# Optimization experiments

Hardware: AMD Instinct MI355X
Metric: run time of the kernel (lower is better)

## Reference

```python
import jax, jax.numpy as jnp
import numpy as np

B, T, H, L = 256, 1024, 64, 5  # batch, seq_len, hidden_size, num_layers


def setup_inputs() -> dict:
    key = jax.random.key(0)
    ks = jax.random.split(key, 10)
    s = 1.0 / np.sqrt(H)  # PyTorch LSTM/Linear uniform init bound

    def u(k, shape):
        return jax.random.uniform(k, shape, jnp.float32, -s, s)

    return {
        "x": jax.random.normal(ks[0], (B, T, 1), jnp.float32),
        "w_ih0": u(ks[1], (4 * H, 1)),          # layer 0 input weights (input_size=1)
        "w_ih_rest": u(ks[2], (L - 1, 4 * H, H)),  # layers 1..4 input weights
        "w_hh": u(ks[3], (L, 4 * H, H)),
        "b_ih": u(ks[4], (L, 4 * H)),
        "b_hh": u(ks[5], (L, 4 * H)),
        "W1": u(ks[6], (H, H)),
        "b1": u(ks[7], (H,)),
        "W2": u(ks[8], (1, H)),
        "b2": u(ks[9], (1,)),
        "future": 0,
    }


def _lstm_layer(x, w_ih, w_hh, b_ih, b_hh):
    # x: [B, T, in]; PyTorch gate order i, f, g, o
    gx = jnp.einsum('bti,gi->btg', x, w_ih) + b_ih  # precompute input projections [B,T,4H]
    h0 = jnp.zeros((x.shape[0], w_hh.shape[1]), x.dtype)

    def step(carry, gxt):
        h, c = carry
        gates = gxt + h @ w_hh.T + b_hh  # [B,4H]
        i, f, g, o = jnp.split(gates, 4, axis=-1)
        c = jax.nn.sigmoid(f) * c + jax.nn.sigmoid(i) * jnp.tanh(g)
        h = jax.nn.sigmoid(o) * jnp.tanh(c)
        return (h, c), h

    _, hs = jax.lax.scan(step, (h0, h0), jnp.swapaxes(gx, 0, 1))  # scan over time
    return jnp.swapaxes(hs, 0, 1)  # [B,T,H]


def _model(x, w_ih0, w_ih_rest, w_hh, b_ih, b_hh, W1, b1, W2, b2):
    # 5-layer LSTM (inter-layer dropout=0.1 is inactive in eval mode)
    h = _lstm_layer(x, w_ih0, w_hh[0], b_ih[0], b_hh[0])
    for l in range(1, w_hh.shape[0]):
        h = _lstm_layer(h, w_ih_rest[l - 1], w_hh[l], b_ih[l], b_hh[l])
    h = jax.nn.relu(h)
    h = jax.nn.relu(h @ W1.T + b1)
    return h @ W2.T + b2  # [B,T,1]


def reference(x, w_ih0, w_ih_rest, w_hh, b_ih, b_hh, W1, b1, W2, b2, future):
    out = None
    for _ in range(future + 1):
        out = _model(x, w_ih0, w_ih_rest, w_hh, b_ih, b_hh, W1, b1, W2, b2)
        x = jnp.concatenate([x, out[:, -1:, :]], axis=1)
    return out
```

## Files before the change

kernel.cpp:

```cpp
#include <hip/hip_runtime.h>

#define B_ 256
#define T_ 1024
#define H_ 64

typedef float f32x2 __attribute__((ext_vector_type(2)));
typedef float f32x4 __attribute__((ext_vector_type(4)));

__device__ __forceinline__ float fast_sigmoid(float x) {
    float e = __builtin_amdgcn_exp2f(-1.4426950408889634f * x);
    return __builtin_amdgcn_rcpf(1.0f + e);
}
__device__ __forceinline__ float fast_tanh(float x) {
    float e = __builtin_amdgcn_exp2f(2.8853900817779268f * x);
    return 1.0f - 2.0f * __builtin_amdgcn_rcpf(1.0f + e);
}

template<int CTRL>
__device__ __forceinline__ float dpp_addf(float v) {
    int vi = __builtin_bit_cast(int, v);
    int sh = __builtin_amdgcn_update_dpp(0, vi, CTRL, 0xF, 0xF, true);
    return v + __builtin_bit_cast(float, sh);
}

__device__ __forceinline__ f32x2 lo4(f32x4 v) { return __builtin_shufflevector(v, v, 0, 1); }
__device__ __forceinline__ f32x2 hi4(f32x4 v) { return __builtin_shufflevector(v, v, 2, 3); }

__device__ __forceinline__ void block_sync_lds() {
    asm volatile("s_waitcnt lgkmcnt(0)\n\ts_barrier" ::: "memory");
}

__device__ __forceinline__ float hsum4(f32x4 v) {
    return (v.x + v.y) + (v.z + v.w);
}

__device__ __forceinline__ void dot4x16(const f32x4 wt[4][4],
                                        f32x4 h0, f32x4 h1, f32x4 h2, f32x4 h3,
                                        float acc[4]) {
    #pragma unroll
    for (int r = 0; r < 4; ++r) {
        f32x2 a = {0.f, 0.f}, d = {0.f, 0.f};
        a = __builtin_elementwise_fma(lo4(wt[r][0]), lo4(h0), a);
        d = __builtin_elementwise_fma(hi4(wt[r][0]), hi4(h0), d);
        a = __builtin_elementwise_fma(lo4(wt[r][1]), lo4(h1), a);
        d = __builtin_elementwise_fma(hi4(wt[r][1]), hi4(h1), d);
        a = __builtin_elementwise_fma(lo4(wt[r][2]), lo4(h2), a);
        d = __builtin_elementwise_fma(hi4(wt[r][2]), hi4(h2), d);
        a = __builtin_elementwise_fma(lo4(wt[r][3]), lo4(h3), a);
        d = __builtin_elementwise_fma(hi4(wt[r][3]), hi4(h3), d);
        f32x2 s = a + d;
        acc[r] = s.x + s.y;
    }
}

__global__ __attribute__((amdgpu_flat_work_group_size(768, 768)))
void lstm_pair01(const float* __restrict__ xA,
                 float* __restrict__ hB_out,
                 const float* __restrict__ wA_ih,
                 const float* __restrict__ wA_hh,
                 const float* __restrict__ bA_ih,
                 const float* __restrict__ bA_hh,
                 const float* __restrict__ wB_ih,
                 const float* __restrict__ wB_hh,
                 const float* __restrict__ bB_ih,
                 const float* __restrict__ bB_hh)
{
    const int b   = blockIdx.x;
    const int tid = threadIdx.x;
    const bool isB = (tid < 512);

    __shared__ __align__(16) float xhA[2][80];
    __shared__ __align__(16) float xhB[2][160];

    int kc, j;
    f32x4 wt[4][4];
    float bias0 = 0.f, bias1 = 0.f, bias2 = 0.f, bias3 = 0.f;
    float w00 = 0.f, w01 = 0.f, w02 = 0.f, w03 = 0.f;

    if (isB) {
        kc = tid & 7; j = tid >> 3;
        #pragma unroll
        for (int r = 0; r < 4; ++r) {
            const int row = r * H_ + j;
            const float* base = (kc < 4) ? (wB_ih + row * H_ + kc * 16)
                                         : (wB_hh + row * H_ + (kc - 4) * 16);
            #pragma unroll
            for (int q = 0; q < 4; ++q) wt[r][q] = *(const f32x4*)(base + 4 * q);
        }
        if (kc == 0) {
            bias0 = bB_ih[0*H_+j] + bB_hh[0*H_+j];
            bias1 = bB_ih[1*H_+j] + bB_hh[1*H_+j];
            bias2 = bB_ih[2*H_+j] + bB_hh[2*H_+j];
            bias3 = bB_ih[3*H_+j] + bB_hh[3*H_+j];
        }
    } else {
        const int t2 = tid - 512;
        kc = t2 & 3; j = t2 >> 2;
        #pragma unroll
        for (int r = 0; r < 4; ++r) {
            const int row = r * H_ + j;
            const float* base = wA_hh + row * H_ + kc * 16;
            #pragma unroll
            for (int q = 0; q < 4; ++q) wt[r][q] = *(const f32x4*)(base + 4 * q);
        }
        if (kc == 0) {
            bias0 = bA_ih[0*H_+j] + bA_hh[0*H_+j];
            bias1 = bA_ih[1*H_+j] + bA_hh[1*H_+j];
            bias2 = bA_ih[2*H_+j] + bA_hh[2*H_+j];
            bias3 = bA_ih[3*H_+j] + bA_hh[3*H_+j];
            w00 = wA_ih[0*H_+j]; w01 = wA_ih[1*H_+j];
            w02 = wA_ih[2*H_+j]; w03 = wA_ih[3*H_+j];
        }
    }
    #pragma unroll
    for (int r = 0; r < 4; ++r)
        #pragma unroll
        for (int q = 0; q < 4; ++q)
            asm volatile("" : "+v"(wt[r][q]));

    float c_st = 0.f;
    float xt = (!isB) ? xA[(long)b * T_] : 0.f;

    if (isB) {
        if (tid < H_) xhB[1][80 + (tid >> 4) * 20 + (tid & 15)] = 0.f;
    } else {
        const int t2 = tid - 512;
        if (t2 < H_) xhA[0][(t2 >> 4) * 20 + (t2 & 15)] = 0.f;
    }
    block_sync_lds();

    for (int s = 0; s <= T_; ++s) {
        const int rb = s & 1, wb = rb ^ 1;

        if (isB) {
            if (s >= 1) {
                const f32x4* xv = (const f32x4*)&xhB[rb][kc * 20];
                f32x4 h0 = xv[0], h1 = xv[1], h2 = xv[2], h3 = xv[3];
                float acc[4];
                dot4x16(wt, h0, h1, h2, h3, acc);
                acc[0] = dpp_addf<0xB1>(acc[0]); acc[1] = dpp_addf<0xB1>(acc[1]);
                acc[2] = dpp_addf<0xB1>(acc[2]); acc[3] = dpp_addf<0xB1>(acc[3]);
                acc[0] = dpp_addf<0x4E>(acc[0]); acc[1] = dpp_addf<0x4E>(acc[1]);
                acc[2] = dpp_addf<0x4E>(acc[2]); acc[3] = dpp_addf<0x4E>(acc[3]);
                acc[0] = dpp_addf<0x141>(acc[0]); acc[1] = dpp_addf<0x141>(acc[1]);
                acc[2] = dpp_addf<0x141>(acc[2]); acc[3] = dpp_addf<0x141>(acc[3]);
                if (kc == 0) {
                    float i_ = fast_sigmoid(acc[0] + bias0);
                    float f_ = fast_sigmoid(acc[1] + bias1);
                    float g_ = fast_tanh   (acc[2] + bias2);
                    float o_ = fast_sigmoid(acc[3] + bias3);
                    c_st = f_ * c_st + i_ * g_;
                    float h = o_ * fast_tanh(c_st);
                    xhB[wb][80 + (j >> 4) * 20 + (j & 15)] = h;
                    hB_out[((long)b * T_ + (s - 1)) * H_ + j] = h;
                }
            }
        } else {
            if (s < T_) {
                float xn = 0.f;
                if (s + 1 < T_) xn = xA[(long)b * T_ + s + 1];
                const f32x4* xv = (const f32x4*)&xhA[rb][kc * 20];
                f32x4 h0 = xv[0], h1 = xv[1], h2 = xv[2], h3 = xv[3];
                float acc[4];
                dot4x16(wt, h0, h1, h2, h3, acc);
                acc[0] = dpp_addf<0xB1>(acc[0]); acc[1] = dpp_addf<0xB1>(acc[1]);
                acc[2] = dpp_addf<0xB1>(acc[2]); acc[3] = dpp_addf<0xB1>(acc[3]);
                acc[0] = dpp_addf<0x4E>(acc[0]); acc[1] = dpp_addf<0x4E>(acc[1]);
                acc[2] = dpp_addf<0x4E>(acc[2]); acc[3] = dpp_addf<0x4E>(acc[3]);
                if (kc == 0) {
                    float gi = acc[0] + bias0 + w00 * xt;
                    float gf = acc[1] + bias1 + w01 * xt;
                    float gg = acc[2] + bias2 + w02 * xt;
                    float go = acc[3] + bias3 + w03 * xt;
                    float i_ = fast_sigmoid(gi);
                    float f_ = fast_sigmoid(gf);
                    float g_ = fast_tanh(gg);
                    float o_ = fast_sigmoid(go);
                    c_st = f_ * c_st + i_ * g_;
                    float h = o_ * fast_tanh(c_st);
                    const int off = (j >> 4) * 20 + (j & 15);
                    xhA[wb][off] = h;
                    xhB[wb][off] = h;
                }
                xt = xn;
            }
        }
        block_sync_lds();
    }
}

__global__ __attribute__((amdgpu_flat_work_group_size(768, 768)))
void lstm_triple(const float* xin,
                 float* hout,
                 const float* __restrict__ wP_ih, const float* __restrict__ wP_hh,
                 const float* __restrict__ bP_ih, const float* __restrict__ bP_hh,
                 const float* __restrict__ wM_ih, const float* __restrict__ wM_hh,
                 const float* __restrict__ bM_ih, const float* __restrict__ bM_hh,
                 const float* __restrict__ wZ_ih, const float* __restrict__ wZ_hh,
                 const float* __restrict__ bZ_ih, const float* __restrict__ bZ_hh)
{
    const int b    = blockIdx.x;
    const int tid  = threadIdx.x;
    const int role = tid >> 8;
    const int loc  = tid & 255;
    const int kc   = loc & 3;
    const int j    = loc >> 2;

    __shared__ __align__(16) float bufP[2][144];
    __shared__ __align__(16) float bufM[2][144];
    __shared__ __align__(16) float bufZ[2][144];

    const float* w_ih = (role == 0) ? wP_ih : (role == 1) ? wM_ih : wZ_ih;
    const float* w_hh = (role == 0) ? wP_hh : (role == 1) ? wM_hh : wZ_hh;
    const float* b_ih = (role == 0) ? bP_ih : (role == 1) ? bM_ih : bZ_ih;
    const float* b_hh = (role == 0) ? bP_hh : (role == 1) ? bM_hh : bZ_hh;
    float (*myBuf)[144] = (role == 0) ? bufP : (role == 1) ? bufM : bufZ;
    float (*dnBuf)[144] = (role == 0) ? bufM : (role == 1) ? bufZ : bufP;

    f32x4 wt[4][8];
    #pragma unroll
    for (int r = 0; r < 4; ++r) {
        const int row = r * H_ + j;
        const float* base = (kc < 2) ? (w_ih + row * H_ + kc * 32)
                                     : (w_hh + row * H_ + (kc - 2) * 32);
        #pragma unroll
        for (int q = 0; q < 8; ++q)
            wt[r][q] = *(const f32x4*)(base + 4 * q);
    }
    #pragma unroll
    for (int r = 0; r < 4; ++r)
        #pragma unroll
        for (int q = 0; q < 8; ++q)
            asm volatile("" : "+v"(wt[r][q]));

    float bias0 = 0.f, bias1 = 0.f, bias2 = 0.f, bias3 = 0.f;
    if (kc == 0) {
        bias0 = b_ih[0*H_+j] + b_hh[0*H_+j];
        bias1 = b_ih[1*H_+j] + b_hh[1*H_+j];
        bias2 = b_ih[2*H_+j] + b_hh[2*H_+j];
        bias3 = b_ih[3*H_+j] + b_hh[3*H_+j];
    }
    float c_st = 0.f;

    if (tid < 64) {
        const int u = tid;
        bufP[0][(u >> 5) * 36 + (u & 31)] = xin[(long)b * T_ * H_ + u];
        bufP[0][((u >> 5) + 2) * 36 + (u & 31)] = 0.f;
    } else if (tid < 128) {
        const int u = tid - 64;
        bufM[1][((u >> 5) + 2) * 36 + (u & 31)] = 0.f;
    } else if (tid < 192) {
        const int u = tid - 128;
        bufZ[0][((u >> 5) + 2) * 36 + (u & 31)] = 0.f;
    }
    block_sync_lds();

    for (int s = 0; s <= T_ + 1; ++s) {
        const int rb = s & 1, wb = rb ^ 1;
        const bool active = (role == 0) ? (s < T_)
                          : (role == 1) ? (s >= 1 && s <= T_)
                                        : (s >= 2);
        if (active) {
            float xn = 0.f;
            if (role == 0 && kc == 1 && s + 1 < T_)
                xn = xin[((long)b * T_ + s + 1) * H_ + j];

            const f32x4* xv = (const f32x4*)&myBuf[rb][kc * 36];
            f32x4 a0 = {0,0,0,0}, a1 = {0,0,0,0}, a2 = {0,0,0,0}, a3 = {0,0,0,0};
            #pragma unroll
            for (int q = 0; q < 8; ++q) {
                f32x4 hq = xv[q];
                a0 = __builtin_elementwise_fma(wt[0][q], hq, a0);
                a1 = __builtin_elementwise_fma(wt[1][q], hq, a1);
                a2 = __builtin_elementwise_fma(wt[2][q], hq, a2);
                a3 = __builtin_elementwise_fma(wt[3][q], hq, a3);
            }
            float acc0 = hsum4(a0), acc1 = hsum4(a1);
            float acc2 = hsum4(a2), acc3 = hsum4(a3);

            acc0 = dpp_addf<0xB1>(acc0); acc1 = dpp_addf<0xB1>(acc1);
            acc2 = dpp_addf<0xB1>(acc2); acc3 = dpp_addf<0xB1>(acc3);
            acc0 = dpp_addf<0x4E>(acc0); acc1 = dpp_addf<0x4E>(acc1);
            acc2 = dpp_addf<0x4E>(acc2); acc3 = dpp_addf<0x4E>(acc3);

            if (kc == 0) {
                float i_ = fast_sigmoid(acc0 + bias0);
                float f_ = fast_sigmoid(acc1 + bias1);
                float g_ = fast_tanh   (acc2 + bias2);
                float o_ = fast_sigmoid(acc3 + bias3);
                c_st = f_ * c_st + i_ * g_;
                float h = o_ * fast_tanh(c_st);
                const int hoff = ((j >> 5) + 2) * 36 + (j & 31);
                const int xoff = (j >> 5) * 36 + (j & 31);
                myBuf[wb][hoff] = h;
                if (role < 2) dnBuf[wb][xoff] = h;
                else          hout[((long)b * T_ + (s - 2)) * H_ + j] = h;
            }
            if (role == 0 && kc == 1)
                bufP[wb][(j >> 5) * 36 + (j & 31)] = xn;
        }
        block_sync_lds();
    }
}

__global__ __launch_bounds__(256)
void mlp_head_v2(const float* __restrict__ hbuf,
                 const float* __restrict__ W1,
                 const float* __restrict__ b1,
                 const float* __restrict__ W2,
                 const float* __restrict__ b2,
                 float* __restrict__ out)
{
    const long r = (long)blockIdx.x * 256 + threadIdx.x;

    float row[H_];
    const float4* src = (const float4*)(hbuf + r * H_);
    #pragma unroll
    for (int q = 0; q < 16; ++q) {
        float4 v = src[q];
        row[4*q+0] = fmaxf(v.x, 0.f); row[4*q+1] = fmaxf(v.y, 0.f);
        row[4*q+2] = fmaxf(v.z, 0.f); row[4*q+3] = fmaxf(v.w, 0.f);
    }
    #pragma unroll
    for (int q = 0; q < 16; ++q)
        asm volatile("" : "+v"(row[4*q]), "+v"(row[4*q+1]),
                         "+v"(row[4*q+2]), "+v"(row[4*q+3]));

    float acc = b2[0];
    for (int jj = 0; jj < H_; ++jj) {
        const float* wrow = W1 + jj * H_;
        float s0 = 0.f, s1 = 0.f, s2 = 0.f, s3 = 0.f;
        #pragma unroll
        for (int q = 0; q < 16; ++q) {
            s0 += row[4*q+0] * wrow[4*q+0];
            s1 += row[4*q+1] * wrow[4*q+1];
            s2 += row[4*q+2] * wrow[4*q+2];
            s3 += row[4*q+3] * wrow[4*q+3];
        }
        float y = fmaxf(b1[jj] + (s0 + s1) + (s2 + s3), 0.f);
        acc += y * W2[jj];
    }
    out[r] = acc;
}

extern "C" void kernel_launch(void* const* d_in, const int* in_sizes, int n_in,
                              void* d_out, int out_size, void* d_ws, size_t ws_size,
                              hipStream_t stream) {
    const float* x     = (const float*)d_in[0];
    const float* w_ih0 = (const float*)d_in[1];
    const float* w_ihr = (const float*)d_in[2];
    const float* w_hh  = (const float*)d_in[3];
    const float* b_ih  = (const float*)d_in[4];
    const float* b_hh  = (const float*)d_in[5];
    const float* W1    = (const float*)d_in[6];
    const float* b1    = (const float*)d_in[7];
    const float* W2    = (const float*)d_in[8];
    const float* b2    = (const float*)d_in[9];

    float* out = (float*)d_out;
    float* buf = (float*)d_ws;

    const long LW = 4L * H_ * H_;
    const long LB = 4L * H_;

    lstm_pair01<<<dim3(B_), dim3(768), 0, stream>>>(
        x, buf,
        w_ih0,          w_hh + 0 * LW, b_ih + 0 * LB, b_hh + 0 * LB,
        w_ihr + 0 * LW, w_hh + 1 * LW, b_ih + 1 * LB, b_hh + 1 * LB);

    lstm_triple<<<dim3(B_), dim3(768), 0, stream>>>(
        buf, buf,
        w_ihr + 1 * LW, w_hh + 2 * LW, b_ih + 2 * LB, b_hh + 2 * LB,
        w_ihr + 2 * LW, w_hh + 3 * LW, b_ih + 3 * LB, b_hh + 3 * LB,
        w_ihr + 3 * LW, w_hh + 4 * LW, b_ih + 4 * LB, b_hh + 4 * LB);

    mlp_head_v2<<<dim3((B_ * T_) / 256), dim3(256), 0, stream>>>(
        buf, W1, b1, W2, b2, out);
}
```

Baseline: 1.752 ms.

## Split LSTM dot product over eight lanes with two hidden units per lane group

Changes the lstm_triple work split so each hidden-unit pair is computed by 8 lanes, each covering a 16-wide K chunk, instead of 4 lanes each covering 32 elements for one unit. The aim is to shorten the serial FMA chain and LDS read per lane on the per-timestep critical path, at the cost of an extra DPP reduction stage and more gate work per output lane. LDS buffers are re-laid out with 20-float row stride, and writes of h and x become 2-wide vector stores. Register count for weights is unchanged.

```diff
diff --git a/kernel.cpp b/kernel.cpp
--- a/kernel.cpp
+++ b/kernel.cpp
@@ -23,16 +23,13 @@
     return v + __builtin_bit_cast(float, sh);
 }
 
+__device__ __forceinline__ void block_sync_lds() {
+    asm volatile("s_waitcnt lgkmcnt(0)\n\ts_barrier" ::: "memory");
+}
+
 __device__ __forceinline__ f32x2 lo4(f32x4 v) { return __builtin_shufflevector(v, v, 0, 1); }
 __device__ __forceinline__ f32x2 hi4(f32x4 v) { return __builtin_shufflevector(v, v, 2, 3); }
-
-__device__ __forceinline__ void block_sync_lds() {
-    asm volatile("s_waitcnt lgkmcnt(0)\n\ts_barrier" ::: "memory");
-}
-
-__device__ __forceinline__ float hsum4(f32x4 v) {
-    return (v.x + v.y) + (v.z + v.w);
-}
+__device__ __forceinline__ float hsum4(f32x4 v) { return (v.x + v.y) + (v.z + v.w); }
 
 __device__ __forceinline__ void dot4x16(const f32x4 wt[4][4],
                                         f32x4 h0, f32x4 h1, f32x4 h2, f32x4 h3,
@@ -190,8 +187,8 @@
 }
 
 __global__ __attribute__((amdgpu_flat_work_group_size(768, 768)))
-void lstm_triple(const float* xin,
-                 float* hout,
+void lstm_triple(const float* __restrict__ xin,
+                 float* __restrict__ hout,
                  const float* __restrict__ wP_ih, const float* __restrict__ wP_hh,
                  const float* __restrict__ bP_ih, const float* __restrict__ bP_hh,
                  const float* __restrict__ wM_ih, const float* __restrict__ wM_hh,
@@ -203,55 +200,75 @@
     const int tid  = threadIdx.x;
     const int role = tid >> 8;
     const int loc  = tid & 255;
-    const int kc   = loc & 3;
-    const int j    = loc >> 2;
-
-    __shared__ __align__(16) float bufP[2][144];
-    __shared__ __align__(16) float bufM[2][144];
-    __shared__ __align__(16) float bufZ[2][144];
+    const int kc   = loc & 7;
+    const int u2   = loc >> 3;
+
+    __shared__ __align__(16) float bufP[2][160];
+    __shared__ __align__(16) float bufM[2][160];
+    __shared__ __align__(16) float bufZ[2][160];
 
     const float* w_ih = (role == 0) ? wP_ih : (role == 1) ? wM_ih : wZ_ih;
     const float* w_hh = (role == 0) ? wP_hh : (role == 1) ? wM_hh : wZ_hh;
     const float* b_ih = (role == 0) ? bP_ih : (role == 1) ? bM_ih : bZ_ih;
     const float* b_hh = (role == 0) ? bP_hh : (role == 1) ? bM_hh : bZ_hh;
-    float (*myBuf)[144] = (role == 0) ? bufP : (role == 1) ? bufM : bufZ;
-    float (*dnBuf)[144] = (role == 0) ? bufM : (role == 1) ? bufZ : bufP;
-
-    f32x4 wt[4][8];
-    #pragma unroll
-    for (int r = 0; r < 4; ++r) {
-        const int row = r * H_ + j;
-        const float* base = (kc < 2) ? (w_ih + row * H_ + kc * 32)
-                                     : (w_hh + row * H_ + (kc - 2) * 32);
-        #pragma unroll
-        for (int q = 0; q < 8; ++q)
-            wt[r][q] = *(const f32x4*)(base + 4 * q);
-    }
+    float (*myBuf)[160] = (role == 0) ? bufP : (role == 1) ? bufM : bufZ;
+    float (*dnBuf)[160] = (role == 0) ? bufM : (role == 1) ? bufZ : bufP;
+
+    f32x4 wtA[4][4], wtB[4][4];
+    #pragma unroll
+    for (int g = 0; g < 2; ++g)
+        #pragma unroll
+        for (int p = 0; p < 2; ++p) {
+            const int row = g * H_ + 2 * u2 + p;
+            const float* base = (kc < 4) ? (w_ih + row * H_ + kc * 16)
+                                         : (w_hh + row * H_ + (kc - 4) * 16);
+            #pragma unroll
+            for (int q = 0; q < 4; ++q)
+                wtA[g * 2 + p][q] = *(const f32x4*)(base + 4 * q);
+        }
+    #pragma unroll
+    for (int g = 2; g < 4; ++g)
+        #pragma unroll
+        for (int p = 0; p < 2; ++p) {
+            const int row = g * H_ + 2 * u2 + p;
+            const float* base = (kc < 4) ? (w_ih + row * H_ + kc * 16)
+                                         : (w_hh + row * H_ + (kc - 4) * 16);
+            #pragma unroll
+            for (int q = 0; q < 4; ++q)
+                wtB[(g - 2) * 2 + p][q] = *(const f32x4*)(base + 4 * q);
+        }
     #pragma unroll
     for (int r = 0; r < 4; ++r)
         #pragma unroll
-        for (int q = 0; q < 8; ++q)
-            asm volatile("" : "+v"(wt[r][q]));
-
-    float bias0 = 0.f, bias1 = 0.f, bias2 = 0.f, bias3 = 0.f;
+        for (int q = 0; q < 4; ++q) {
+            asm volatile("" : "+v"(wtA[r][q]));
+            asm volatile("" : "+v"(wtB[r][q]));
+        }
+
+    float bias[8];
+    #pragma unroll
+    for (int r = 0; r < 8; ++r) bias[r] = 0.f;
     if (kc == 0) {
-        bias0 = b_ih[0*H_+j] + b_hh[0*H_+j];
-        bias1 = b_ih[1*H_+j] + b_hh[1*H_+j];
-        bias2 = b_ih[2*H_+j] + b_hh[2*H_+j];
-        bias3 = b_ih[3*H_+j] + b_hh[3*H_+j];
-    }
-    float c_st = 0.f;
-
-    if (tid < 64) {
+        #pragma unroll
+        for (int g = 0; g < 4; ++g)
+            #pragma unroll
+            for (int p = 0; p < 2; ++p) {
+                const int row = g * H_ + 2 * u2 + p;
+                bias[g * 2 + p] = b_ih[row] + b_hh[row];
+            }
+    }
+    float c0 = 0.f, c1 = 0.f;
+
+    if (tid < H_) {
         const int u = tid;
-        bufP[0][(u >> 5) * 36 + (u & 31)] = xin[(long)b * T_ * H_ + u];
-        bufP[0][((u >> 5) + 2) * 36 + (u & 31)] = 0.f;
+        bufP[0][(u >> 4) * 20 + (u & 15)] = xin[(long)b * T_ * H_ + u];
+        bufP[0][(4 + (u >> 4)) * 20 + (u & 15)] = 0.f;
     } else if (tid < 128) {
         const int u = tid - 64;
-        bufM[1][((u >> 5) + 2) * 36 + (u & 31)] = 0.f;
+        bufM[1][(4 + (u >> 4)) * 20 + (u & 15)] = 0.f;
     } else if (tid < 192) {
         const int u = tid - 128;
-        bufZ[0][((u >> 5) + 2) * 36 + (u & 31)] = 0.f;
+        bufZ[0][(4 + (u >> 4)) * 20 + (u & 15)] = 0.f;
     }
     block_sync_lds();
 
@@ -261,43 +278,94 @@
                           : (role == 1) ? (s >= 1 && s <= T_)
                                         : (s >= 2);
         if (active) {
-            float xn = 0.f;
+            f32x2 xn = {0.f, 0.f};
             if (role == 0 && kc == 1 && s + 1 < T_)
-                xn = xin[((long)b * T_ + s + 1) * H_ + j];
-
-            const f32x4* xv = (const f32x4*)&myBuf[rb][kc * 36];
-            f32x4 a0 = {0,0,0,0}, a1 = {0,0,0,0}, a2 = {0,0,0,0}, a3 = {0,0,0,0};
-            #pragma unroll
-            for (int q = 0; q < 8; ++q) {
-                f32x4 hq = xv[q];
-                a0 = __builtin_elementwise_fma(wt[0][q], hq, a0);
-                a1 = __builtin_elementwise_fma(wt[1][q], hq, a1);
-                a2 = __builtin_elementwise_fma(wt[2][q], hq, a2);
-                a3 = __builtin_elementwise_fma(wt[3][q], hq, a3);
-            }
-            float acc0 = hsum4(a0), acc1 = hsum4(a1);
-            float acc2 = hsum4(a2), acc3 = hsum4(a3);
-
-            acc0 = dpp_addf<0xB1>(acc0); acc1 = dpp_addf<0xB1>(acc1);
-            acc2 = dpp_addf<0xB1>(acc2); acc3 = dpp_addf<0xB1>(acc3);
-            acc0 = dpp_addf<0x4E>(acc0); acc1 = dpp_addf<0x4E>(acc1);
-            acc2 = dpp_addf<0x4E>(acc2); acc3 = dpp_addf<0x4E>(acc3);
+                xn = *(const f32x2*)&xin[((long)b * T_ + s + 1) * H_ + 2 * u2];
+
+            const f32x4* xv = (const f32x4*)&myBuf[rb][kc * 20];
+            f32x4 ch0 = xv[0], ch1 = xv[1], ch2 = xv[2], ch3 = xv[3];
+
+            float red[8];
+            {
+                f32x4 a0 = {0,0,0,0}, a1 = {0,0,0,0}, a2 = {0,0,0,0}, a3 = {0,0,0,0};
+                a0 = __builtin_elementwise_fma(wtA[0][0], ch0, a0);
+                a1 = __builtin_elementwise_fma(wtA[1][0], ch0, a1);
+                a2 = __builtin_elementwise_fma(wtA[2][0], ch0, a2);
+                a3 = __builtin_elementwise_fma(wtA[3][0], ch0, a3);
+                a0 = __builtin_elementwise_fma(wtA[0][1], ch1, a0);
+                a1 = __builtin_elementwise_fma(wtA[1][1], ch1, a1);
+                a2 = __builtin_elementwise_fma(wtA[2][1], ch1, a2);
+                a3 = __builtin_elementwise_fma(wtA[3][1], ch1, a3);
+                a0 = __builtin_elementwise_fma(wtA[0][2], ch2, a0);
+                a1 = __builtin_elementwise_fma(wtA[1][2], ch2, a1);
+                a2 = __builtin_elementwise_fma(wtA[2][2], ch2, a2);
+                a3 = __builtin_elementwise_fma(wtA[3][2], ch2, a3);
+                a0 = __builtin_elementwise_fma(wtA[0][3], ch3, a0);
+                a1 = __builtin_elementwise_fma(wtA[1][3], ch3, a1);
+                a2 = __builtin_elementwise_fma(wtA[2][3], ch3, a2);
+                a3 = __builtin_elementwise_fma(wtA[3][3], ch3, a3);
+                red[0] = hsum4(a0); red[1] = hsum4(a1);
+                red[2] = hsum4(a2); red[3] = hsum4(a3);
+            }
+            {
+                f32x4 a0 = {0,0,0,0}, a1 = {0,0,0,0}, a2 = {0,0,0,0}, a3 = {0,0,0,0};
+                a0 = __builtin_elementwise_fma(wtB[0][0], ch0, a0);
+                a1 = __builtin_elementwise_fma(wtB[1][0], ch0, a1);
+                a2 = __builtin_elementwise_fma(wtB[2][0], ch0, a2);
+                a3 = __builtin_elementwise_fma(wtB[3][0], ch0, a3);
+                a0 = __builtin_elementwise_fma(wtB[0][1], ch1, a0);
+                a1 = __builtin_elementwise_fma(wtB[1][1], ch1, a1);
+                a2 = __builtin_elementwise_fma(wtB[2][1], ch1, a2);
+                a3 = __builtin_elementwise_fma(wtB[3][1], ch1, a3);
+                a0 = __builtin_elementwise_fma(wtB[0][2], ch2, a0);
+                a1 = __builtin_elementwise_fma(wtB[1][2], ch2, a1);
+                a2 = __builtin_elementwise_fma(wtB[2][2], ch2, a2);
+                a3 = __builtin_elementwise_fma(wtB[3][2], ch2, a3);
+                a0 = __builtin_elementwise_fma(wtB[0][3], ch3, a0);
+                a1 = __builtin_elementwise_fma(wtB[1][3], ch3, a1);
+                a2 = __builtin_elementwise_fma(wtB[2][3], ch3, a2);
+                a3 = __builtin_elementwise_fma(wtB[3][3], ch3, a3);
+                red[4] = hsum4(a0); red[5] = hsum4(a1);
+                red[6] = hsum4(a2); red[7] = hsum4(a3);
+            }
+
+            #pragma unroll
+            for (int r = 0; r < 8; ++r) red[r] = dpp_addf<0xB1>(red[r]);
+            #pragma unroll
+            for (int r = 0; r < 8; ++r) red[r] = dpp_addf<0x4E>(red[r]);
+            #pragma unroll
+            for (int r = 0; r < 8; ++r) red[r] = dpp_addf<0x141>(red[r]);
 
             if (kc == 0) {
-                float i_ = fast_sigmoid(acc0 + bias0);
-                float f_ = fast_sigmoid(acc1 + bias1);
-                float g_ = fast_tanh   (acc2 + bias2);
-                float o_ = fast_sigmoid(acc3 + bias3);
-                c_st = f_ * c_st + i_ * g_;
-                float h = o_ * fast_tanh(c_st);
-                const int hoff = ((j >> 5) + 2) * 36 + (j & 31);
-                const int xoff = (j >> 5) * 36 + (j & 31);
-                myBuf[wb][hoff] = h;
-                if (role < 2) dnBuf[wb][xoff] = h;
-                else          hout[((long)b * T_ + (s - 2)) * H_ + j] = h;
-            }
-            if (role == 0 && kc == 1)
-                bufP[wb][(j >> 5) * 36 + (j & 31)] = xn;
+                float h0v, h1v;
+                {
+                    float i_ = fast_sigmoid(red[0] + bias[0]);
+                    float f_ = fast_sigmoid(red[2] + bias[2]);
+                    float g_ = fast_tanh   (red[4] + bias[4]);
+                    float o_ = fast_sigmoid(red[6] + bias[6]);
+                    c0 = f_ * c0 + i_ * g_;
+                    h0v = o_ * fast_tanh(c0);
+                }
+                {
+                    float i_ = fast_sigmoid(red[1] + bias[1]);
+                    float f_ = fast_sigmoid(red[3] + bias[3]);
+                    float g_ = fast_tanh   (red[5] + bias[5]);
+                    float o_ = fast_sigmoid(red[7] + bias[7]);
+                    c1 = f_ * c1 + i_ * g_;
+                    h1v = o_ * fast_tanh(c1);
+                }
+                const int u = 2 * u2;
+                const f32x2 hp = {h0v, h1v};
+                *(f32x2*)&myBuf[wb][(4 + (u >> 4)) * 20 + (u & 15)] = hp;
+                if (role < 2)
+                    *(f32x2*)&dnBuf[wb][(u >> 4) * 20 + (u & 15)] = hp;
+                else
+                    *(f32x2*)&hout[((long)b * T_ + (s - 2)) * H_ + u] = hp;
+            }
+            if (role == 0 && kc == 1) {
+                const int u = 2 * u2;
+                *(f32x2*)&bufP[wb][(u >> 4) * 20 + (u & 15)] = xn;
+            }
         }
         block_sync_lds();
     }
```

New measurement: 2.498 ms. 1.43x slower.

## Regroup LSTM layers into a 0-1-2 triple kernel and a 3-4 pair kernel

Applied to the files above, without the earlier changes.

Layers are rebalanced across the two wavefront-pipelined kernels. The first kernel now runs layers 0, 1 and 2 with 256 threads each (768 total). The second kernel runs layers 3 and 4 with 512 threads. Layer 1 switches from 8-way to 4-way K-splitting with 32-element chunks, which removes one DPP reduction stage. This shortens the combined serial step chain of the two kernels but adds more FMA work per thread, and the second kernel uses fewer threads per block.

```diff
diff --git a/kernel.cpp b/kernel.cpp
--- a/kernel.cpp
+++ b/kernel.cpp
@@ -23,127 +23,173 @@
     return v + __builtin_bit_cast(float, sh);
 }
 
-__device__ __forceinline__ f32x2 lo4(f32x4 v) { return __builtin_shufflevector(v, v, 0, 1); }
-__device__ __forceinline__ f32x2 hi4(f32x4 v) { return __builtin_shufflevector(v, v, 2, 3); }
-
 __device__ __forceinline__ void block_sync_lds() {
     asm volatile("s_waitcnt lgkmcnt(0)\n\ts_barrier" ::: "memory");
 }
 
-__device__ __forceinline__ float hsum4(f32x4 v) {
-    return (v.x + v.y) + (v.z + v.w);
-}
-
-__device__ __forceinline__ void dot4x16(const f32x4 wt[4][4],
-                                        f32x4 h0, f32x4 h1, f32x4 h2, f32x4 h3,
+__device__ __forceinline__ float hsum4(f32x4 v) { return (v.x + v.y) + (v.z + v.w); }
+
+__device__ __forceinline__ void load_w_heavy(const float* __restrict__ w_ih,
+                                             const float* __restrict__ w_hh,
+                                             int j, int kc, f32x4 wt[4][8]) {
+    #pragma unroll
+    for (int r = 0; r < 4; ++r) {
+        const int row = r * H_ + j;
+        const float* base = (kc < 2) ? (w_ih + row * H_ + kc * 32)
+                                     : (w_hh + row * H_ + (kc - 2) * 32);
+        #pragma unroll
+        for (int q = 0; q < 8; ++q)
+            wt[r][q] = *(const f32x4*)(base + 4 * q);
+    }
+    #pragma unroll
+    for (int r = 0; r < 4; ++r)
+        #pragma unroll
+        for (int q = 0; q < 8; ++q)
+            asm volatile("" : "+v"(wt[r][q]));
+}
+
+__device__ __forceinline__ void dot4x32(const float* chunk, const f32x4 wt[4][8],
                                         float acc[4]) {
-    #pragma unroll
-    for (int r = 0; r < 4; ++r) {
-        f32x2 a = {0.f, 0.f}, d = {0.f, 0.f};
-        a = __builtin_elementwise_fma(lo4(wt[r][0]), lo4(h0), a);
-        d = __builtin_elementwise_fma(hi4(wt[r][0]), hi4(h0), d);
-        a = __builtin_elementwise_fma(lo4(wt[r][1]), lo4(h1), a);
-        d = __builtin_elementwise_fma(hi4(wt[r][1]), hi4(h1), d);
-        a = __builtin_elementwise_fma(lo4(wt[r][2]), lo4(h2), a);
-        d = __builtin_elementwise_fma(hi4(wt[r][2]), hi4(h2), d);
-        a = __builtin_elementwise_fma(lo4(wt[r][3]), lo4(h3), a);
-        d = __builtin_elementwise_fma(hi4(wt[r][3]), hi4(h3), d);
-        f32x2 s = a + d;
-        acc[r] = s.x + s.y;
-    }
+    const f32x4* xv = (const f32x4*)chunk;
+    f32x4 a0 = {0,0,0,0}, a1 = {0,0,0,0}, a2 = {0,0,0,0}, a3 = {0,0,0,0};
+    #pragma unroll
+    for (int q = 0; q < 8; ++q) {
+        f32x4 hq = xv[q];
+        a0 = __builtin_elementwise_fma(wt[0][q], hq, a0);
+        a1 = __builtin_elementwise_fma(wt[1][q], hq, a1);
+        a2 = __builtin_elementwise_fma(wt[2][q], hq, a2);
+        a3 = __builtin_elementwise_fma(wt[3][q], hq, a3);
+    }
+    acc[0] = hsum4(a0); acc[1] = hsum4(a1);
+    acc[2] = hsum4(a2); acc[3] = hsum4(a3);
 }
 
 __global__ __attribute__((amdgpu_flat_work_group_size(768, 768)))
-void lstm_pair01(const float* __restrict__ xA,
-                 float* __restrict__ hB_out,
-                 const float* __restrict__ wA_ih,
-                 const float* __restrict__ wA_hh,
-                 const float* __restrict__ bA_ih,
-                 const float* __restrict__ bA_hh,
-                 const float* __restrict__ wB_ih,
-                 const float* __restrict__ wB_hh,
-                 const float* __restrict__ bB_ih,
-                 const float* __restrict__ bB_hh)
+void lstm_tri012(const float* __restrict__ x,
+                 float* __restrict__ hout,
+                 const float* __restrict__ w_ih0,
+                 const float* __restrict__ whh0,
+                 const float* __restrict__ bih0, const float* __restrict__ bhh0,
+                 const float* __restrict__ wih1, const float* __restrict__ whh1,
+                 const float* __restrict__ bih1, const float* __restrict__ bhh1,
+                 const float* __restrict__ wih2, const float* __restrict__ whh2,
+                 const float* __restrict__ bih2, const float* __restrict__ bhh2)
 {
-    const int b   = blockIdx.x;
-    const int tid = threadIdx.x;
-    const bool isB = (tid < 512);
-
-    __shared__ __align__(16) float xhA[2][80];
-    __shared__ __align__(16) float xhB[2][160];
-
-    int kc, j;
-    f32x4 wt[4][4];
+    const int b    = blockIdx.x;
+    const int tid  = threadIdx.x;
+    const int role = tid >> 8;
+    const int loc  = tid & 255;
+    const int kc   = loc & 3;
+    const int j    = loc >> 2;
+
+    __shared__ __align__(16) float bufL0[2][80];
+    __shared__ __align__(16) float bufL1[2][144];
+    __shared__ __align__(16) float bufL2[2][144];
+
+    f32x4 wt[4][8];
     float bias0 = 0.f, bias1 = 0.f, bias2 = 0.f, bias3 = 0.f;
     float w00 = 0.f, w01 = 0.f, w02 = 0.f, w03 = 0.f;
 
-    if (isB) {
-        kc = tid & 7; j = tid >> 3;
+    if (role == 0) {
         #pragma unroll
         for (int r = 0; r < 4; ++r) {
             const int row = r * H_ + j;
-            const float* base = (kc < 4) ? (wB_ih + row * H_ + kc * 16)
-                                         : (wB_hh + row * H_ + (kc - 4) * 16);
+            const float* base = whh0 + row * H_ + kc * 16;
             #pragma unroll
-            for (int q = 0; q < 4; ++q) wt[r][q] = *(const f32x4*)(base + 4 * q);
-        }
+            for (int q = 0; q < 4; ++q)
+                wt[r][q] = *(const f32x4*)(base + 4 * q);
+        }
+        #pragma unroll
+        for (int r = 0; r < 4; ++r)
+            #pragma unroll
+            for (int q = 0; q < 4; ++q)
+                asm volatile("" : "+v"(wt[r][q]));
         if (kc == 0) {
-            bias0 = bB_ih[0*H_+j] + bB_hh[0*H_+j];
-            bias1 = bB_ih[1*H_+j] + bB_hh[1*H_+j];
-            bias2 = bB_ih[2*H_+j] + bB_hh[2*H_+j];
-            bias3 = bB_ih[3*H_+j] + bB_hh[3*H_+j];
+            bias0 = bih0[0*H_+j] + bhh0[0*H_+j];
+            bias1 = bih0[1*H_+j] + bhh0[1*H_+j];
+            bias2 = bih0[2*H_+j] + bhh0[2*H_+j];
+            bias3 = bih0[3*H_+j] + bhh0[3*H_+j];
+            w00 = w_ih0[0*H_+j]; w01 = w_ih0[1*H_+j];
+            w02 = w_ih0[2*H_+j]; w03 = w_ih0[3*H_+j];
         }
     } else {
-        const int t2 = tid - 512;
-        kc = t2 & 3; j = t2 >> 2;
-        #pragma unroll
-        for (int r = 0; r < 4; ++r) {
-            const int row = r * H_ + j;
-            const float* base = wA_hh + row * H_ + kc * 16;
-            #pragma unroll
-            for (int q = 0; q < 4; ++q) wt[r][q] = *(const f32x4*)(base + 4 * q);
-        }
+        const float* wih = (role == 1) ? wih1 : wih2;
+        const float* whh = (role == 1) ? whh1 : whh2;
+        const float* bih = (role == 1) ? bih1 : bih2;
+        const float* bhh = (role == 1) ? bhh1 : bhh2;
+        load_w_heavy(wih, whh, j, kc, wt);
         if (kc == 0) {
-            bias0 = bA_ih[0*H_+j] + bA_hh[0*H_+j];
-            bias1 = bA_ih[1*H_+j] + bA_hh[1*H_+j];
-            bias2 = bA_ih[2*H_+j] + bA_hh[2*H_+j];
-            bias3 = bA_ih[3*H_+j] + bA_hh[3*H_+j];
-            w00 = wA_ih[0*H_+j]; w01 = wA_ih[1*H_+j];
-            w02 = wA_ih[2*H_+j]; w03 = wA_ih[3*H_+j];
-        }
-    }
-    #pragma unroll
-    for (int r = 0; r < 4; ++r)
-        #pragma unroll
-        for (int q = 0; q < 4; ++q)
-            asm volatile("" : "+v"(wt[r][q]));
-
+            bias0 = bih[0*H_+j] + bhh[0*H_+j];
+            bias1 = bih[1*H_+j] + bhh[1*H_+j];
+            bias2 = bih[2*H_+j] + bhh[2*H_+j];
+            bias3 = bih[3*H_+j] + bhh[3*H_+j];
+        }
+    }
     float c_st = 0.f;
-    float xt = (!isB) ? xA[(long)b * T_] : 0.f;
-
-    if (isB) {
-        if (tid < H_) xhB[1][80 + (tid >> 4) * 20 + (tid & 15)] = 0.f;
-    } else {
-        const int t2 = tid - 512;
-        if (t2 < H_) xhA[0][(t2 >> 4) * 20 + (t2 & 15)] = 0.f;
+    float xt = (role == 0) ? x[(long)b * T_] : 0.f;
+
+    float (*myBuf)[144] = (role == 1) ? bufL1 : bufL2;
+
+    if (loc < H_) {
+        const int u = loc;
+        if (role == 0)      bufL0[0][(u >> 4) * 20 + (u & 15)] = 0.f;
+        else if (role == 1) bufL1[1][(2 + (u >> 5)) * 36 + (u & 31)] = 0.f;
+        else                bufL2[0][(2 + (u >> 5)) * 36 + (u & 31)] = 0.f;
     }
     block_sync_lds();
 
-    for (int s = 0; s <= T_; ++s) {
+    for (int s = 0; s <= T_ + 1; ++s) {
         const int rb = s & 1, wb = rb ^ 1;
-
-        if (isB) {
-            if (s >= 1) {
-                const f32x4* xv = (const f32x4*)&xhB[rb][kc * 20];
+        const bool active = (role == 0) ? (s < T_)
+                          : (role == 1) ? (s >= 1 && s <= T_)
+                                        : (s >= 2);
+        if (active) {
+            if (role == 0) {
+                float xn = 0.f;
+                if (s + 1 < T_) xn = x[(long)b * T_ + s + 1];
+                const f32x4* xv = (const f32x4*)&bufL0[rb][kc * 20];
                 f32x4 h0 = xv[0], h1 = xv[1], h2 = xv[2], h3 = xv[3];
+                f32x4 a0 = {0,0,0,0}, a1 = {0,0,0,0}, a2 = {0,0,0,0}, a3 = {0,0,0,0};
+                a0 = __builtin_elementwise_fma(wt[0][0], h0, a0);
+                a1 = __builtin_elementwise_fma(wt[1][0], h0, a1);
+                a2 = __builtin_elementwise_fma(wt[2][0], h0, a2);
+                a3 = __builtin_elementwise_fma(wt[3][0], h0, a3);
+                a0 = __builtin_elementwise_fma(wt[0][1], h1, a0);
+                a1 = __builtin_elementwise_fma(wt[1][1], h1, a1);
+                a2 = __builtin_elementwise_fma(wt[2][1], h1, a2);
+                a3 = __builtin_elementwise_fma(wt[3][1], h1, a3);
+                a0 = __builtin_elementwise_fma(wt[0][2], h2, a0);
+                a1 = __builtin_elementwise_fma(wt[1][2], h2, a1);
+                a2 = __builtin_elementwise_fma(wt[2][2], h2, a2);
+                a3 = __builtin_elementwise_fma(wt[3][2], h2, a3);
+                a0 = __builtin_elementwise_fma(wt[0][3], h3, a0);
+                a1 = __builtin_elementwise_fma(wt[1][3], h3, a1);
+                a2 = __builtin_elementwise_fma(wt[2][3], h3, a2);
+                a3 = __builtin_elementwise_fma(wt[3][3], h3, a3);
+                float acc0 = hsum4(a0), acc1 = hsum4(a1);
+                float acc2 = hsum4(a2), acc3 = hsum4(a3);
+                acc0 = dpp_addf<0xB1>(acc0); acc1 = dpp_addf<0xB1>(acc1);
+                acc2 = dpp_addf<0xB1>(acc2); acc3 = dpp_addf<0xB1>(acc3);
+                acc0 = dpp_addf<0x4E>(acc0); acc1 = dpp_addf<0x4E>(acc1);
+                acc2 = dpp_addf<0x4E>(acc2); acc3 = dpp_addf<0x4E>(acc3);
+                if (kc == 0) {
+                    float i_ = fast_sigmoid(acc0 + bias0 + w00 * xt);
+                    float f_ = fast_sigmoid(acc1 + bias1 + w01 * xt);
+                    float g_ = fast_tanh   (acc2 + bias2 + w02 * xt);
+                    float o_ = fast_sigmoid(acc3 + bias3 + w03 * xt);
+                    c_st = f_ * c_st + i_ * g_;
+                    float h = o_ * fast_tanh(c_st);
+                    bufL0[wb][(j >> 4) * 20 + (j & 15)] = h;
+                    bufL1[wb][(j >> 5) * 36 + (j & 31)] = h;
+                }
+                xt = xn;
+            } else {
                 float acc[4];
-                dot4x16(wt, h0, h1, h2, h3, acc);
+                dot4x32(&myBuf[rb][kc * 36], wt, acc);
                 acc[0] = dpp_addf<0xB1>(acc[0]); acc[1] = dpp_addf<0xB1>(acc[1]);
                 acc[2] = dpp_addf<0xB1>(acc[2]); acc[3] = dpp_addf<0xB1>(acc[3]);
                 acc[0] = dpp_addf<0x4E>(acc[0]); acc[1] = dpp_addf<0x4E>(acc[1]);
                 acc[2] = dpp_addf<0x4E>(acc[2]); acc[3] = dpp_addf<0x4E>(acc[3]);
-                acc[0] = dpp_addf<0x141>(acc[0]); acc[1] = dpp_addf<0x141>(acc[1]);
-                acc[2] = dpp_addf<0x141>(acc[2]); acc[3] = dpp_addf<0x141>(acc[3]);
                 if (kc == 0) {
                     float i_ = fast_sigmoid(acc[0] + bias0);
                     float f_ = fast_sigmoid(acc[1] + bias1);
@@ -151,53 +197,25 @@
                     float o_ = fast_sigmoid(acc[3] + bias3);
                     c_st = f_ * c_st + i_ * g_;
                     float h = o_ * fast_tanh(c_st);
-                    xhB[wb][80 + (j >> 4) * 20 + (j & 15)] = h;
-                    hB_out[((long)b * T_ + (s - 1)) * H_ + j] = h;
+                    myBuf[wb][(2 + (j >> 5)) * 36 + (j & 31)] = h;
+                    if (role == 1)
+                        bufL2[wb][(j >> 5) * 36 + (j & 31)] = h;
+                    else
+                        hout[((long)b * T_ + (s - 2)) * H_ + j] = h;
                 }
             }
-        } else {
-            if (s < T_) {
-                float xn = 0.f;
-                if (s + 1 < T_) xn = xA[(long)b * T_ + s + 1];
-                const f32x4* xv = (const f32x4*)&xhA[rb][kc * 20];
-                f32x4 h0 = xv[0], h1 = xv[1], h2 = xv[2], h3 = xv[3];
-                float acc[4];
-                dot4x16(wt, h0, h1, h2, h3, acc);
-                acc[0] = dpp_addf<0xB1>(acc[0]); acc[1] = dpp_addf<0xB1>(acc[1]);
-                acc[2] = dpp_addf<0xB1>(acc[2]); acc[3] = dpp_addf<0xB1>(acc[3]);
-                acc[0] = dpp_addf<0x4E>(acc[0]); acc[1] = dpp_addf<0x4E>(acc[1]);
-                acc[2] = dpp_addf<0x4E>(acc[2]); acc[3] = dpp_addf<0x4E>(acc[3]);
-                if (kc == 0) {
-                    float gi = acc[0] + bias0 + w00 * xt;
-                    float gf = acc[1] + bias1 + w01 * xt;
-                    float gg = acc[2] + bias2 + w02 * xt;
-                    float go = acc[3] + bias3 + w03 * xt;
-                    float i_ = fast_sigmoid(gi);
-                    float f_ = fast_sigmoid(gf);
-                    float g_ = fast_tanh(gg);
-                    float o_ = fast_sigmoid(go);
-                    c_st = f_ * c_st + i_ * g_;
-                    float h = o_ * fast_tanh(c_st);
-                    const int off = (j >> 4) * 20 + (j & 15);
-                    xhA[wb][off] = h;
-                    xhB[wb][off] = h;
-                }
-                xt = xn;
-            }
         }
         block_sync_lds();
     }
 }
 
-__global__ __attribute__((amdgpu_flat_work_group_size(768, 768)))
-void lstm_triple(const float* xin,
-                 float* hout,
-                 const float* __restrict__ wP_ih, const float* __restrict__ wP_hh,
-                 const float* __restrict__ bP_ih, const float* __restrict__ bP_hh,
-                 const float* __restrict__ wM_ih, const float* __restrict__ wM_hh,
-                 const float* __restrict__ bM_ih, const float* __restrict__ bM_hh,
-                 const float* __restrict__ wZ_ih, const float* __restrict__ wZ_hh,
-                 const float* __restrict__ bZ_ih, const float* __restrict__ bZ_hh)
+__global__ __attribute__((amdgpu_flat_work_group_size(512, 512)))
+void lstm_pair34(const float* __restrict__ xin,
+                 float* __restrict__ hout,
+                 const float* __restrict__ wih3, const float* __restrict__ whh3,
+                 const float* __restrict__ bih3, const float* __restrict__ bhh3,
+                 const float* __restrict__ wih4, const float* __restrict__ whh4,
+                 const float* __restrict__ bih4, const float* __restrict__ bhh4)
 {
     const int b    = blockIdx.x;
     const int tid  = threadIdx.x;
@@ -206,98 +224,67 @@
     const int kc   = loc & 3;
     const int j    = loc >> 2;
 
-    __shared__ __align__(16) float bufP[2][144];
-    __shared__ __align__(16) float bufM[2][144];
-    __shared__ __align__(16) float bufZ[2][144];
-
-    const float* w_ih = (role == 0) ? wP_ih : (role == 1) ? wM_ih : wZ_ih;
-    const float* w_hh = (role == 0) ? wP_hh : (role == 1) ? wM_hh : wZ_hh;
-    const float* b_ih = (role == 0) ? bP_ih : (role == 1) ? bM_ih : bZ_ih;
-    const float* b_hh = (role == 0) ? bP_hh : (role == 1) ? bM_hh : bZ_hh;
-    float (*myBuf)[144] = (role == 0) ? bufP : (role == 1) ? bufM : bufZ;
-    float (*dnBuf)[144] = (role == 0) ? bufM : (role == 1) ? bufZ : bufP;
+    __shared__ __align__(16) float bufL3[2][144];
+    __shared__ __align__(16) float bufL4[2][144];
+
+    const float* wih = (role == 0) ? wih3 : wih4;
+    const float* whh = (role == 0) ? whh3 : whh4;
+    const float* bih = (role == 0) ? bih3 : bih4;
+    const float* bhh = (role == 0) ? bhh3 : bhh4;
+    float (*myBuf)[144] = (role == 0) ? bufL3 : bufL4;
 
     f32x4 wt[4][8];
-    #pragma unroll
-    for (int r = 0; r < 4; ++r) {
-        const int row = r * H_ + j;
-        const float* base = (kc < 2) ? (w_ih + row * H_ + kc * 32)
-                                     : (w_hh + row * H_ + (kc - 2) * 32);
-        #pragma unroll
-        for (int q = 0; q < 8; ++q)
-            wt[r][q] = *(const f32x4*)(base + 4 * q);
-    }
-    #pragma unroll
-    for (int r = 0; r < 4; ++r)
-        #pragma unroll
-        for (int q = 0; q < 8; ++q)
-            asm volatile("" : "+v"(wt[r][q]));
+    load_w_heavy(wih, whh, j, kc, wt);
 
     float bias0 = 0.f, bias1 = 0.f, bias2 = 0.f, bias3 = 0.f;
     if (kc == 0) {
-        bias0 = b_ih[0*H_+j] + b_hh[0*H_+j];
-        bias1 = b_ih[1*H_+j] + b_hh[1*H_+j];
-        bias2 = b_ih[2*H_+j] + b_hh[2*H_+j];
-        bias3 = b_ih[3*H_+j] + b_hh[3*H_+j];
+        bias0 = bih[0*H_+j] + bhh[0*H_+j];
+        bias1 = bih[1*H_+j] + bhh[1*H_+j];
+        bias2 = bih[2*H_+j] + bhh[2*H_+j];
+        bias3 = bih[3*H_+j] + bhh[3*H_+j];
     }
     float c_st = 0.f;
 
-    if (tid < 64) {
+    if (tid < H_) {
         const int u = tid;
-        bufP[0][(u >> 5) * 36 + (u & 31)] = xin[(long)b * T_ * H_ + u];
-        bufP[0][((u >> 5) + 2) * 36 + (u & 31)] = 0.f;
+        bufL3[0][(u >> 5) * 36 + (u & 31)] = xin[(long)b * T_ * H_ + u];
+        bufL3[0][(2 + (u >> 5)) * 36 + (u & 31)] = 0.f;
     } else if (tid < 128) {
         const int u = tid - 64;
-        bufM[1][((u >> 5) + 2) * 36 + (u & 31)] = 0.f;
-    } else if (tid < 192) {
-        const int u = tid - 128;
-        bufZ[0][((u >> 5) + 2) * 36 + (u & 31)] = 0.f;
+        bufL4[1][(2 + (u >> 5)) * 36 + (u & 31)] = 0.f;
     }
     block_sync_lds();
 
-    for (int s = 0; s <= T_ + 1; ++s) {
+    for (int s = 0; s <= T_; ++s) {
         const int rb = s & 1, wb = rb ^ 1;
-        const bool active = (role == 0) ? (s < T_)
-                          : (role == 1) ? (s >= 1 && s <= T_)
-                                        : (s >= 2);
+        const bool active = (role == 0) ? (s < T_) : (s >= 1);
         if (active) {
             float xn = 0.f;
             if (role == 0 && kc == 1 && s + 1 < T_)
                 xn = xin[((long)b * T_ + s + 1) * H_ + j];
 
-            const f32x4* xv = (const f32x4*)&myBuf[rb][kc * 36];
-            f32x4 a0 = {0,0,0,0}, a1 = {0,0,0,0}, a2 = {0,0,0,0}, a3 = {0,0,0,0};
-            #pragma unroll
-            for (int q = 0; q < 8; ++q) {
-                f32x4 hq = xv[q];
-                a0 = __builtin_elementwise_fma(wt[0][q], hq, a0);
-                a1 = __builtin_elementwise_fma(wt[1][q], hq, a1);
-                a2 = __builtin_elementwise_fma(wt[2][q], hq, a2);
-                a3 = __builtin_elementwise_fma(wt[3][q], hq, a3);
-            }
-            float acc0 = hsum4(a0), acc1 = hsum4(a1);
-            float acc2 = hsum4(a2), acc3 = hsum4(a3);
-
-            acc0 = dpp_addf<0xB1>(acc0); acc1 = dpp_addf<0xB1>(acc1);
-            acc2 = dpp_addf<0xB1>(acc2); acc3 = dpp_addf<0xB1>(acc3);
-            acc0 = dpp_addf<0x4E>(acc0); acc1 = dpp_addf<0x4E>(acc1);
-            acc2 = dpp_addf<0x4E>(acc2); acc3 = dpp_addf<0x4E>(acc3);
+            float acc[4];
+            dot4x32(&myBuf[rb][kc * 36], wt, acc);
+            acc[0] = dpp_addf<0xB1>(acc[0]); acc[1] = dpp_addf<0xB1>(acc[1]);
+            acc[2] = dpp_addf<0xB1>(acc[2]); acc[3] = dpp_addf<0xB1>(acc[3]);
+            acc[0] = dpp_addf<0x4E>(acc[0]); acc[1] = dpp_addf<0x4E>(acc[1]);
+            acc[2] = dpp_addf<0x4E>(acc[2]); acc[3] = dpp_addf<0x4E>(acc[3]);
 
             if (kc == 0) {
-                float i_ = fast_sigmoid(acc0 + bias0);
-                float f_ = fast_sigmoid(acc1 + bias1);
-                float g_ = fast_tanh   (acc2 + bias2);
-                float o_ = fast_sigmoid(acc3 + bias3);
+                float i_ = fast_sigmoid(acc[0] + bias0);
+                float f_ = fast_sigmoid(acc[1] + bias1);
+                float g_ = fast_tanh   (acc[2] + bias2);
+                float o_ = fast_sigmoid(acc[3] + bias3);
                 c_st = f_ * c_st + i_ * g_;
                 float h = o_ * fast_tanh(c_st);
-                const int hoff = ((j >> 5) + 2) * 36 + (j & 31);
-                const int xoff = (j >> 5) * 36 + (j & 31);
-                myBuf[wb][hoff] = h;
-                if (role < 2) dnBuf[wb][xoff] = h;
-                else          hout[((long)b * T_ + (s - 2)) * H_ + j] = h;
+                myBuf[wb][(2 + (j >> 5)) * 36 + (j & 31)] = h;
+                if (role == 0)
+                    bufL4[wb][(j >> 5) * 36 + (j & 31)] = h;
+                else
+                    hout[((long)b * T_ + (s - 1)) * H_ + j] = h;
             }
             if (role == 0 && kc == 1)
-                bufP[wb][(j >> 5) * 36 + (j & 31)] = xn;
+                bufL3[wb][(j >> 5) * 36 + (j & 31)] = xn;
         }
         block_sync_lds();
     }
@@ -363,14 +350,14 @@
     const long LW = 4L * H_ * H_;
     const long LB = 4L * H_;
 
-    lstm_pair01<<<dim3(B_), dim3(768), 0, stream>>>(
+    lstm_tri012<<<dim3(B_), dim3(768), 0, stream>>>(
         x, buf,
-        w_ih0,          w_hh + 0 * LW, b_ih + 0 * LB, b_hh + 0 * LB,
-        w_ihr + 0 * LW, w_hh + 1 * LW, b_ih + 1 * LB, b_hh + 1 * LB);
-
-    lstm_triple<<<dim3(B_), dim3(768), 0, stream>>>(
+        w_ih0, w_hh + 0 * LW, b_ih + 0 * LB, b_hh + 0 * LB,
+        w_ihr + 0 * LW, w_hh + 1 * LW, b_ih + 1 * LB, b_hh + 1 * LB,
+        w_ihr + 1 * LW, w_hh + 2 * LW, b_ih + 2 * LB, b_hh + 2 * LB);
+
+    lstm_pair34<<<dim3(B_), dim3(512), 0, stream>>>(
         buf, buf,
-        w_ihr + 1 * LW, w_hh + 2 * LW, b_ih + 2 * LB, b_hh + 2 * LB,
         w_ihr + 2 * LW, w_hh + 3 * LW, b_ih + 3 * LB, b_hh + 3 * LB,
         w_ihr + 3 * LW, w_hh + 4 * LW, b_ih + 4 * LB, b_hh + 4 * LB);
 
```

Measured after the change: 1.713 ms, median of 2. 2.2% less time.
